# Kernel optimization log

Measured on AMD Instinct MI355X. Metric: run time of the kernel, lower is better.

## Reference

```python
import jax, jax.numpy as jnp
import numpy as np

N = 30        # samples per curve
W = 60        # image width/height
LENGTH = 160  # curves per sample
ALPHA = 0.0002
VIEWBOX = (0.0, 0.0, 1.0, 1.0)


def _bezier_basis(n):
    # Warped parameter t, then cubic Bernstein-like basis, shape (n, 4)
    t = jnp.arange(n, dtype=jnp.float32) / n
    t = 2 * t**3 - 3 * t**2 + 2 * t
    t_bar = 1 - t
    t_3_0 = t**3
    t_2_1 = t**2 - t_3_0
    t_1_2 = t_3_0 - 2 * t**2 + t
    t_0_3 = t_bar**3
    return jnp.stack([t_3_0, 3 * t_2_1, 3 * t_1_2, t_0_3], axis=1)


def setup_inputs() -> dict:
    key = jax.random.key(0)
    x = jax.random.uniform(key, (256, LENGTH, 8), dtype=jnp.float32)
    return {"x": x}


def reference(x) -> jnp.ndarray:
    B, L = x.shape[0], x.shape[1]
    T = _bezier_basis(N)                                   # (n, 4)
    ctrl = x.reshape(B, L, 4, 2)                           # 4 control points (x,y)
    points = jnp.einsum('nk,blkc->blnc', T, ctrl)          # (B, L, n, 2)
    X = points[..., 0]                                     # (B, L, n)
    Y = points[..., 1]
    board = jnp.arange(W, dtype=jnp.float32) / W           # (w,)
    bx = board * VIEWBOX[2] + VIEWBOX[0]
    by = board * VIEWBOX[3] + VIEWBOX[1]
    # Gaussian splats along each axis: (B, L, w, n)
    gx = jnp.exp(-jnp.square(bx[None, None, :, None] - X[:, :, None, :]) / ALPHA)
    gy = jnp.exp(-jnp.square(by[None, None, :, None] - Y[:, :, None, :]) / ALPHA)
    # Outer product over sample points n, summed over curves L: (B, w, w)
    result = jnp.einsum('blin,bljn->bij', gx, gy)
    return jnp.minimum(result, 1.0)
```

## Files before the change

### kernel.cpp

```cpp
#include <hip/hip_runtime.h>


#define WIDTH 60
#define LCURVES 160
#define NSAMP 30
#define NEG_INVA_LOG2E (-7213.4752f)

typedef _Float16 half8 __attribute__((ext_vector_type(8)));
typedef float floatx4 __attribute__((ext_vector_type(4)));

__global__ __launch_bounds__(256) void bezier_mfma_kernel(
    const float* __restrict__ x, float* __restrict__ out) {
    __shared__ __align__(16) char smem[65536];

    const int tid = threadIdx.x;
    const int lane = tid & 63;
    const int w = tid >> 6;
    const int b = blockIdx.x;
    const int m = lane & 15;
    const int q = lane >> 4;

    float4* sz = (float4*)smem;
#pragma unroll
    for (int i = 0; i < 16; ++i)
        sz[tid + 256 * i] = make_float4(0.f, 0.f, 0.f, 0.f);
    __syncthreads();

    _Float16* gx = (_Float16*)(smem + w * 16384);
    _Float16* gy = gx + 4096;

    floatx4 acc[4][4];
#pragma unroll
    for (int ti = 0; ti < 4; ++ti)
#pragma unroll
        for (int tj = 0; tj < 4; ++tj)
            acc[ti][tj] = (floatx4){0.f, 0.f, 0.f, 0.f};

    const float* xb = x + (size_t)b * (LCURVES * 8);
    int prev_i0 = 0, prev_j0 = 0;

    for (int c = w; c < 75; c += 4) {
        int s = c * 64 + lane;
        int l = s % LCURVES;
        int n = s / LCURVES;

        const float4* cp = (const float4*)(xb + l * 8);
        float4 c0 = cp[0];
        float4 c1 = cp[1];

        float tt = (float)n * (1.0f / NSAMP);
        tt = 2.0f * tt * tt * tt - 3.0f * tt * tt + 2.0f * tt;
        float tb = 1.0f - tt, t2 = tt * tt;
        float w0 = t2 * tt;
        float w1 = 3.0f * (t2 - w0);
        float w2 = 3.0f * tt * tb * tb;
        float w3 = tb * tb * tb;
        float X = w0 * c0.x + w1 * c0.z + w2 * c1.x + w3 * c1.z;
        float Y = w0 * c0.y + w1 * c0.w + w2 * c1.y + w3 * c1.w;

        int i0 = (int)floorf(X * (float)WIDTH);
        int j0 = (int)floorf(Y * (float)WIDTH);
        i0 = min(max(i0, 0), 59);
        j0 = min(max(j0, 0), 59);

#pragma unroll
        for (int a = 0; a < 6; ++a) {
            int rz = min(prev_i0 + a, 63);
            gx[rz * 64 + (lane ^ ((rz & 7) << 3))] = (_Float16)0;
            int rz2 = min(prev_j0 + a, 63);
            gy[rz2 * 64 + (lane ^ ((rz2 & 7) << 3))] = (_Float16)0;
        }
        float bx = (float)(i0 - 2) * (1.0f / WIDTH) - X;
        float by = (float)(j0 - 2) * (1.0f / WIDTH) - Y;
#pragma unroll
        for (int a = 0; a < 6; ++a) {
            float dx = bx + (float)a * (1.0f / WIDTH);
            float vx = __builtin_amdgcn_exp2f(dx * dx * NEG_INVA_LOG2E);
            int r = min(i0 + a, 63);
            gx[r * 64 + (lane ^ ((r & 7) << 3))] = (_Float16)vx;
            float dy = by + (float)a * (1.0f / WIDTH);
            float vy = __builtin_amdgcn_exp2f(dy * dy * NEG_INVA_LOG2E);
            int r2 = min(j0 + a, 63);
            gy[r2 * 64 + (lane ^ ((r2 & 7) << 3))] = (_Float16)vy;
        }
        prev_i0 = i0;
        prev_j0 = j0;

#pragma unroll
        for (int kk = 0; kk < 2; ++kk) {
            half8 af[4], bf[4];
#pragma unroll
            for (int t = 0; t < 4; ++t) {
                int ra = t * 16 + m;
                af[t] = *(const half8*)&gx[ra * 64 + (((kk * 4 + q) ^ (ra & 7)) << 3)];
                bf[t] = *(const half8*)&gy[ra * 64 + (((kk * 4 + q) ^ (ra & 7)) << 3)];
            }
#pragma unroll
            for (int ti = 0; ti < 4; ++ti)
#pragma unroll
                for (int tj = 0; tj < 4; ++tj)
                    acc[ti][tj] = __builtin_amdgcn_mfma_f32_16x16x32_f16(
                        af[ti], bf[tj], acc[ti][tj], 0, 0, 0);
        }
    }

    __syncthreads();
    if (w > 0) {
        float* red = (float*)smem + (w - 1) * (64 * 65);
#pragma unroll
        for (int ti = 0; ti < 4; ++ti)
#pragma unroll
            for (int tj = 0; tj < 4; ++tj)
#pragma unroll
                for (int r = 0; r < 4; ++r)
                    red[(ti * 16 + q * 4 + r) * 65 + tj * 16 + m] = acc[ti][tj][r];
    }
    __syncthreads();
    if (w == 0) {
        float* r0 = (float*)smem;
        float* r1 = r0 + 64 * 65;
        float* r2 = r1 + 64 * 65;
        float* ob = out + (size_t)b * (WIDTH * WIDTH);
#pragma unroll
        for (int ti = 0; ti < 4; ++ti)
#pragma unroll
            for (int tj = 0; tj < 4; ++tj)
#pragma unroll
                for (int r = 0; r < 4; ++r) {
                    int row = ti * 16 + q * 4 + r;
                    int col = tj * 16 + m;
                    int i = row - 2, j = col - 2;
                    if ((unsigned)i < WIDTH && (unsigned)j < WIDTH) {
                        float v = acc[ti][tj][r] + r0[row * 65 + col] +
                                  r1[row * 65 + col] + r2[row * 65 + col];
                        ob[i * WIDTH + j] = fminf(v, 1.0f);
                    }
                }
    }
}

extern "C" void kernel_launch(void* const* d_in, const int* in_sizes, int n_in,
                              void* d_out, int out_size, void* d_ws, size_t ws_size,
                              hipStream_t stream) {
    const float* x = (const float*)d_in[0];
    float* out = (float*)d_out;
    int B = in_sizes[0] / (LCURVES * 8);
    bezier_mfma_kernel<<<B, 256, 0, stream>>>(x, out);
}
```

Baseline: 78.47 us.

## Software-pipeline tap computation with MFMA accumulation in Bezier splat kernel

The per-chunk loop is restructured so that all LDS fragment loads for both k-halves are issued first. The next chunk's Bezier point evaluation and Gaussian exp taps are then computed into registers while the current chunk's 32 MFMAs execute, and the LDS tiles are zeroed and rewritten only after the MFMAs. This aims to hide the global loads and ALU/transcendental latency behind the matrix-core work. In exchange it raises register pressure (double fragment arrays plus 12 tap values), which could cut occupancy.

```diff
diff --git a/kernel.cpp b/kernel.cpp
--- a/kernel.cpp
+++ b/kernel.cpp
@@ -8,6 +8,60 @@
 
 typedef _Float16 half8 __attribute__((ext_vector_type(8)));
 typedef float floatx4 __attribute__((ext_vector_type(4)));
+
+#define COMPUTE_TAPS(CARG)                                                \
+    {                                                                     \
+        int s = (CARG) * 64 + lane;                                       \
+        int l = s % LCURVES;                                              \
+        int n = s / LCURVES;                                              \
+        const float4* cp = (const float4*)(xb + l * 8);                   \
+        float4 c0 = cp[0];                               \
+        float4 c1 = cp[1];                               \
+        float tt = (float)n * (1.0f / NSAMP);                             \
+        tt = 2.0f * tt * tt * tt - 3.0f * tt * tt + 2.0f * tt;            \
+        float tb = 1.0f - tt, t2 = tt * tt;                               \
+        float w0 = t2 * tt;                                               \
+        float w1 = 3.0f * (t2 - w0);                                      \
+        float w2 = 3.0f * tt * tb * tb;                                   \
+        float w3 = tb * tb * tb;                                          \
+        float X = w0 * c0.x + w1 * c0.z + w2 * c1.x + w3 * c1.z;          \
+        float Y = w0 * c0.y + w1 * c0.w + w2 * c1.y + w3 * c1.w;          \
+        ni0 = (int)floorf(X * (float)WIDTH);                              \
+        nj0 = (int)floorf(Y * (float)WIDTH);                              \
+        ni0 = min(max(ni0, 0), 59);                                       \
+        nj0 = min(max(nj0, 0), 59);                                       \
+        float bx = (float)(ni0 - 2) * (1.0f / WIDTH) - X;                 \
+        float by = (float)(nj0 - 2) * (1.0f / WIDTH) - Y;                 \
+        _Pragma("unroll")                                                 \
+        for (int a = 0; a < 6; ++a) {                                     \
+            float dx = bx + (float)a * (1.0f / WIDTH);                    \
+            vxs[a] = __builtin_amdgcn_exp2f(dx * dx * NEG_INVA_LOG2E);    \
+            float dy = by + (float)a * (1.0f / WIDTH);                    \
+            vys[a] = __builtin_amdgcn_exp2f(dy * dy * NEG_INVA_LOG2E);    \
+        }                                                                 \
+    }
+
+#define ZERO_TAPS()                                                       \
+    {                                                                     \
+        _Pragma("unroll")                                                 \
+        for (int a = 0; a < 6; ++a) {                                     \
+            int rz = min(pi0 + a, 63);                                    \
+            gx[rz * 64 + (lane ^ ((rz & 7) << 3))] = (_Float16)0;         \
+            int rz2 = min(pj0 + a, 63);                                   \
+            gy[rz2 * 64 + (lane ^ ((rz2 & 7) << 3))] = (_Float16)0;       \
+        }                                                                 \
+    }
+
+#define WRITE_TAPS()                                                      \
+    {                                                                     \
+        _Pragma("unroll")                                                 \
+        for (int a = 0; a < 6; ++a) {                                     \
+            int r = min(ni0 + a, 63);                                     \
+            gx[r * 64 + (lane ^ ((r & 7) << 3))] = (_Float16)vxs[a];      \
+            int r2 = min(nj0 + a, 63);                                    \
+            gy[r2 * 64 + (lane ^ ((r2 & 7) << 3))] = (_Float16)vys[a];    \
+        }                                                                 \
+    }
 
 __global__ __launch_bounds__(256) void bezier_mfma_kernel(
     const float* __restrict__ x, float* __restrict__ out) {
@@ -37,71 +91,46 @@
             acc[ti][tj] = (floatx4){0.f, 0.f, 0.f, 0.f};
 
     const float* xb = x + (size_t)b * (LCURVES * 8);
-    int prev_i0 = 0, prev_j0 = 0;
 
-    for (int c = w; c < 75; c += 4) {
-        int s = c * 64 + lane;
-        int l = s % LCURVES;
-        int n = s / LCURVES;
+    int pi0, pj0, ni0, nj0;
+    float vxs[6], vys[6];
 
-        const float4* cp = (const float4*)(xb + l * 8);
-        float4 c0 = cp[0];
-        float4 c1 = cp[1];
+    COMPUTE_TAPS(w);
+    WRITE_TAPS();
+    pi0 = ni0;
+    pj0 = nj0;
 
-        float tt = (float)n * (1.0f / NSAMP);
-        tt = 2.0f * tt * tt * tt - 3.0f * tt * tt + 2.0f * tt;
-        float tb = 1.0f - tt, t2 = tt * tt;
-        float w0 = t2 * tt;
-        float w1 = 3.0f * (t2 - w0);
-        float w2 = 3.0f * tt * tb * tb;
-        float w3 = tb * tb * tb;
-        float X = w0 * c0.x + w1 * c0.z + w2 * c1.x + w3 * c1.z;
-        float Y = w0 * c0.y + w1 * c0.w + w2 * c1.y + w3 * c1.w;
-
-        int i0 = (int)floorf(X * (float)WIDTH);
-        int j0 = (int)floorf(Y * (float)WIDTH);
-        i0 = min(max(i0, 0), 59);
-        j0 = min(max(j0, 0), 59);
-
+    for (int cc = w;;) {
+        half8 af[2][4], bf[2][4];
 #pragma unroll
-        for (int a = 0; a < 6; ++a) {
-            int rz = min(prev_i0 + a, 63);
-            gx[rz * 64 + (lane ^ ((rz & 7) << 3))] = (_Float16)0;
-            int rz2 = min(prev_j0 + a, 63);
-            gy[rz2 * 64 + (lane ^ ((rz2 & 7) << 3))] = (_Float16)0;
-        }
-        float bx = (float)(i0 - 2) * (1.0f / WIDTH) - X;
-        float by = (float)(j0 - 2) * (1.0f / WIDTH) - Y;
-#pragma unroll
-        for (int a = 0; a < 6; ++a) {
-            float dx = bx + (float)a * (1.0f / WIDTH);
-            float vx = __builtin_amdgcn_exp2f(dx * dx * NEG_INVA_LOG2E);
-            int r = min(i0 + a, 63);
-            gx[r * 64 + (lane ^ ((r & 7) << 3))] = (_Float16)vx;
-            float dy = by + (float)a * (1.0f / WIDTH);
-            float vy = __builtin_amdgcn_exp2f(dy * dy * NEG_INVA_LOG2E);
-            int r2 = min(j0 + a, 63);
-            gy[r2 * 64 + (lane ^ ((r2 & 7) << 3))] = (_Float16)vy;
-        }
-        prev_i0 = i0;
-        prev_j0 = j0;
-
-#pragma unroll
-        for (int kk = 0; kk < 2; ++kk) {
-            half8 af[4], bf[4];
+        for (int kk = 0; kk < 2; ++kk)
 #pragma unroll
             for (int t = 0; t < 4; ++t) {
                 int ra = t * 16 + m;
-                af[t] = *(const half8*)&gx[ra * 64 + (((kk * 4 + q) ^ (ra & 7)) << 3)];
-                bf[t] = *(const half8*)&gy[ra * 64 + (((kk * 4 + q) ^ (ra & 7)) << 3)];
+                af[kk][t] = *(const half8*)&gx[ra * 64 + (((kk * 4 + q) ^ (ra & 7)) << 3)];
+                bf[kk][t] = *(const half8*)&gy[ra * 64 + (((kk * 4 + q) ^ (ra & 7)) << 3)];
             }
+
+        int cn = cc + 4;
+        bool more = (cn < 75);
+        if (more) COMPUTE_TAPS(cn);
+
+#pragma unroll
+        for (int kk = 0; kk < 2; ++kk)
 #pragma unroll
             for (int ti = 0; ti < 4; ++ti)
 #pragma unroll
                 for (int tj = 0; tj < 4; ++tj)
                     acc[ti][tj] = __builtin_amdgcn_mfma_f32_16x16x32_f16(
-                        af[ti], bf[tj], acc[ti][tj], 0, 0, 0);
-        }
+                        af[kk][ti], bf[kk][tj], acc[ti][tj], 0, 0, 0);
+
+        if (!more) break;
+
+        ZERO_TAPS();
+        WRITE_TAPS();
+        pi0 = ni0;
+        pj0 = nj0;
+        cc = cn;
     }
 
     __syncthreads();
```

Result: slower. 81.93 us (+4.4%).
